# Kernel tuning notes

Measured on AMD Instinct MI355X. Metric: run time of the kernel, lower is better.

Reference implementation:

```python
import jax, jax.numpy as jnp
import numpy as np

GS = 7        # grid_size
NB = 2        # num_boxes
NC = 20       # num_classes
THR = 0.5     # NMS threshold (source default)
IMG = 448.0   # max_size used in _encode_outputs


def _nms_keep(boxes, scores, valid, thr):
    """Faithful port of the source's (inverted) greedy NMS.

    Picks the highest-score alive box, keeps it, then RETAINS only boxes
    with IoU >= thr against it (discarding low-overlap ones), repeating.
    Fixed-shape: returns a bool keep-mask of length N.
    """
    N = scores.shape[0]
    x1, y1, x2, y2 = boxes[:, 0], boxes[:, 1], boxes[:, 2], boxes[:, 3]
    areas = (x2 - x1) * (y2 - y1)
    neg = jnp.asarray(-1e30, scores.dtype)
    idx = jnp.arange(N)

    def step(carry, _):
        alive, keep = carry
        any_alive = jnp.any(alive)
        i = jnp.argmax(jnp.where(alive, scores, neg))
        keep = keep | ((idx == i) & any_alive)
        ix1 = jnp.maximum(x1, x1[i]); iy1 = jnp.maximum(y1, y1[i])
        ix2 = jnp.minimum(x2, x2[i]); iy2 = jnp.minimum(y2, y2[i])
        inter = jnp.clip(ix2 - ix1, 0) * jnp.clip(iy2 - iy1, 0)
        iou = inter / (areas[i] + areas - inter)
        new_alive = (alive & (iou >= thr)) & (idx != i)
        alive = jnp.where(any_alive, new_alive, alive)
        return (alive, keep), None

    (_, keep), _ = jax.lax.scan(step, (valid, jnp.zeros(N, bool)), None, length=N)
    return keep


def _forward(x, W, b):
    B = x.shape[0]
    out = (x @ W.T + b).reshape(B, GS, GS, 5 * NB + NC)  # (B,7,7,30)
    cell = 1.0 / GS
    g = jnp.arange(GS, dtype=out.dtype) * cell
    norm_x = g[None, None, :]   # varies along last grid axis (grid_x[r,c]=c)
    norm_y = g[None, :, None]

    labels = out[..., 5 * NB:]                                # (B,7,7,20)
    labels_proba = jnp.argmax(labels, -1).astype(out.dtype)   # class index

    N = B * GS * GS
    labels_flat = labels.reshape(N, NC)

    slot_boxes, slot_scores, slot_valid = [], [], []
    for off in range(0, 5 * NB, 5):
        bx = out[..., off:off + 4]
        sc = out[..., off + 5]                 # faithful off-by-one in source
        valid = (sc * labels_proba) > 0.5      # faithful score*class_index mask
        cx = bx[..., 0] * cell + norm_x
        cy = bx[..., 1] * cell + norm_y
        w_, h_ = bx[..., 2], bx[..., 3]
        X1 = cx - 0.5 * w_; Y1 = cy - 0.5 * h_
        X2 = cx + 0.5 * w_; Y2 = cy + 0.5 * h_
        # NMS applies xywh2xyxy AGAIN on already-xyxy boxes (faithful):
        bb = jnp.stack([X1 - X2 / 2, Y1 - Y2 / 2, X1 + X2 / 2, Y1 + Y2 / 2], -1)
        slot_boxes.append(bb.reshape(N, 4))
        slot_scores.append(sc.reshape(N))
        slot_valid.append(valid.reshape(N))

    boxes = jnp.stack(slot_boxes)     # (NB, N, 4)
    scores = jnp.stack(slot_scores)   # (NB, N)
    valid = jnp.stack(slot_valid)     # (NB, N)

    keep = jax.vmap(_nms_keep, in_axes=(0, 0, 0, None))(boxes, scores, valid, THR)

    labels_all = jnp.broadcast_to(labels_flat[None], (NB, N, NC))
    packed = jnp.concatenate([boxes * IMG, scores[..., None], labels_all], -1)
    return packed * keep[..., None].astype(packed.dtype)  # (NB, N, 25)


def setup_inputs() -> dict:
    key = jax.random.key(0)
    k1, k2, k3 = jax.random.split(key, 3)
    B = 64
    x = jax.random.normal(k1, (B, 2304), jnp.float32)
    W = jax.random.normal(k2, (1470, 2304), jnp.float32) * 0.02
    b = jax.random.normal(k3, (1470,), jnp.float32) * 0.01
    return {"x": x, "W": W, "b": b}


def reference(x, W, b):
    return _forward(x, W, b)
```

## Files before the change

kernel.cpp:

```cpp
#include <hip/hip_runtime.h>

#define B_     64
#define KDIM   2304
#define NCOL   1470
#define NCELL  3136
#define CPAD   1536
#define SPLITK 16
#define KCHUNK 144
#define NSTAGE 9
#define XS     68
#define WSD    100
#define NMS_T  1024
#define QMAX   4
#define OUTSZ  (2 * NCELL * 25)

__global__ __launch_bounds__(256) void gemm_splitk(
    const float* __restrict__ x, const float* __restrict__ W,
    float* __restrict__ partial, float* __restrict__ out)
{
    __shared__ float sx[2][16 * XS];
    __shared__ float sw[2][16 * WSD];

    const int t = threadIdx.x;

    {
        const int gt = (blockIdx.y * 16 + blockIdx.x) * 256 + t;
        if (gt < OUTSZ / 4)
            *(float4*)&out[gt * 4] = make_float4(0.f, 0.f, 0.f, 0.f);
    }

    const int c0  = blockIdx.x * 96;
    const int k0  = blockIdx.y * KCHUNK;
    const int r8  = (t >> 5) << 3;
    const int cgi = t & 31;
    const int kk0 = t & 15;
    const int g0  = t >> 4;

    float acc[8][3];
#pragma unroll
    for (int i = 0; i < 8; ++i)
#pragma unroll
        for (int j = 0; j < 3; ++j) acc[i][j] = 0.f;

    const float* wp[6];
#pragma unroll
    for (int p = 0; p < 6; ++p) {
        int gc = c0 + p * 16 + g0;
        if (gc >= NCOL) gc = NCOL - 1;
        wp[p] = W + (size_t)gc * KDIM + kk0;
    }

    float xr[4], wr[6];
    {
        const int kb = k0;
#pragma unroll
        for (int p = 0; p < 4; ++p) xr[p] = x[(p * 16 + g0) * KDIM + kb + kk0];
#pragma unroll
        for (int p = 0; p < 6; ++p) wr[p] = wp[p][kb];
#pragma unroll
        for (int p = 0; p < 4; ++p) sx[0][kk0 * XS + p * 16 + g0] = xr[p];
#pragma unroll
        for (int p = 0; p < 6; ++p) sw[0][kk0 * WSD + p * 16 + g0] = wr[p];
    }

    for (int s = 0; s < NSTAGE; ++s) {
        const int cb = s & 1;
        if (s + 1 < NSTAGE) {
            const int kb = k0 + ((s + 1) << 4);
#pragma unroll
            for (int p = 0; p < 4; ++p) xr[p] = x[(p * 16 + g0) * KDIM + kb + kk0];
#pragma unroll
            for (int p = 0; p < 6; ++p) wr[p] = wp[p][kb];
        }
        __syncthreads();
        const float* cx = sx[cb];
        const float* cw = sw[cb];
#pragma unroll
        for (int kk = 0; kk < 16; ++kk) {
            const float4 a0 = *(const float4*)&cx[kk * XS + r8];
            const float4 a1 = *(const float4*)&cx[kk * XS + r8 + 4];
            const float w0 = cw[kk * WSD + cgi];
            const float w1 = cw[kk * WSD + cgi + 32];
            const float w2 = cw[kk * WSD + cgi + 64];
            const float av[8] = {a0.x, a0.y, a0.z, a0.w, a1.x, a1.y, a1.z, a1.w};
#pragma unroll
            for (int i = 0; i < 8; ++i) {
                acc[i][0] = fmaf(av[i], w0, acc[i][0]);
                acc[i][1] = fmaf(av[i], w1, acc[i][1]);
                acc[i][2] = fmaf(av[i], w2, acc[i][2]);
            }
        }
        if (s + 1 < NSTAGE) {
#pragma unroll
            for (int p = 0; p < 4; ++p) sx[cb ^ 1][kk0 * XS + p * 16 + g0] = xr[p];
#pragma unroll
            for (int p = 0; p < 6; ++p) sw[cb ^ 1][kk0 * WSD + p * 16 + g0] = wr[p];
        }
    }

    float* pb = partial + (size_t)blockIdx.y * (B_ * CPAD) + c0 + cgi;
#pragma unroll
    for (int i = 0; i < 8; ++i)
#pragma unroll
        for (int p = 0; p < 3; ++p)
            pb[(size_t)(r8 + i) * CPAD + 32 * p] = acc[i][p];
}

__global__ __launch_bounds__(256) void combine_prep(
    const float* __restrict__ partial, const float* __restrict__ bias,
    float* __restrict__ labels, float* __restrict__ boxes,
    float* __restrict__ scores, int* __restrict__ valid)
{
    __shared__ float sa[8][30];
    const int t    = threadIdx.x;
    const int base = blockIdx.x * 8;

    if (t < 240) {
        const int n   = base + t / 30;
        const int col = t % 30;
        const int row = n / 49;
        const int cr  = (n % 49) * 30 + col;
        float s = 0.f;
#pragma unroll
        for (int k = 0; k < SPLITK; ++k)
            s += partial[(size_t)k * (B_ * CPAD) + (size_t)row * CPAD + cr];
        s += bias[cr];
        sa[t / 30][col] = s;
        if (col >= 10) labels[(size_t)n * 20 + (col - 10)] = s;
    }
    __syncthreads();

    if (t < 8) {
        const int n = base + t;
        const float* a = sa[t];
        float mv = a[10]; int mi = 0;
#pragma unroll
        for (int j = 1; j < 20; ++j) {
            float v = a[10 + j];
            if (v > mv) { mv = v; mi = j; }
        }
        const float lp = (float)mi;
        const int gx = n % 7, gy = (n / 7) % 7;
        const float cw = 1.0f / 7.0f;
        const float nx = (float)gx * cw, ny = (float)gy * cw;
#pragma unroll
        for (int sl = 0; sl < 2; ++sl) {
            const int off = 5 * sl;
            const float bx0 = a[off], bx1 = a[off + 1];
            const float w_ = a[off + 2], h_ = a[off + 3];
            const float sc = a[off + 5];
            const float cx = bx0 * cw + nx, cy = bx1 * cw + ny;
            const float X1 = cx - 0.5f * w_, Y1 = cy - 0.5f * h_;
            const float X2 = cx + 0.5f * w_, Y2 = cy + 0.5f * h_;
            const int m = sl * NCELL + n;
            boxes[m * 4 + 0] = X1 - 0.5f * X2;
            boxes[m * 4 + 1] = Y1 - 0.5f * Y2;
            boxes[m * 4 + 2] = X1 + 0.5f * X2;
            boxes[m * 4 + 3] = Y1 + 0.5f * Y2;
            scores[m] = sc;
            valid[m] = (sc * lp > 0.5f) ? 1 : 0;
        }
    }
}

__global__ __launch_bounds__(NMS_T) void nms_pick(
    const float* __restrict__ boxes, const float* __restrict__ scores,
    const int* __restrict__ valid, const float* __restrict__ labels,
    float* __restrict__ out)
{
    __shared__ float sX1[NCELL], sY1[NCELL], sX2[NCELL], sY2[NCELL];
    __shared__ float sSc[NCELL];
    __shared__ int   pickList[NCELL];
    __shared__ float rv[16];
    __shared__ int   rn[16];
    __shared__ int   pickN, npicks;

    const int slot = blockIdx.x;
    const int base = slot * NCELL;
    const int t = threadIdx.x;

    if (t == 0) npicks = 0;
    unsigned am = 0;
#pragma unroll
    for (int q = 0; q < QMAX; ++q) {
        const int n = t + q * NMS_T;
        if (n < NCELL) {
            const float4 bb = *(const float4*)&boxes[(size_t)(base + n) * 4];
            sX1[n] = bb.x; sY1[n] = bb.y; sX2[n] = bb.z; sY2[n] = bb.w;
            sSc[n] = scores[base + n];
            if (valid[base + n]) am |= 1u << q;
        }
    }
    __syncthreads();

    for (;;) {
        float bv = -1e30f; int bn = 0x7fffffff;
#pragma unroll
        for (int q = 0; q < QMAX; ++q)
            if ((am >> q) & 1u) {
                const int n = t + q * NMS_T;
                const float v = sSc[n];
                if (v > bv || (v == bv && n < bn)) { bv = v; bn = n; }
            }
#pragma unroll
        for (int o = 32; o > 0; o >>= 1) {
            const float ov = __shfl_down(bv, o);
            const int   on = __shfl_down(bn, o);
            if (ov > bv || (ov == bv && on < bn)) { bv = ov; bn = on; }
        }
        if ((t & 63) == 0) { rv[t >> 6] = bv; rn[t >> 6] = bn; }
        __syncthreads();
        if (t == 0) {
            float v2 = rv[0]; int n2 = rn[0];
#pragma unroll
            for (int q = 1; q < 16; ++q)
                if (rv[q] > v2 || (rv[q] == v2 && rn[q] < n2)) { v2 = rv[q]; n2 = rn[q]; }
            if (v2 == -1e30f) { pickN = -1; }
            else { pickN = n2; pickList[npicks++] = n2; }
        }
        __syncthreads();
        const int pn = pickN;
        if (pn < 0) break;
        const float px1 = sX1[pn], py1 = sY1[pn], px2 = sX2[pn], py2 = sY2[pn];
        const float pa = (px2 - px1) * (py2 - py1);

#pragma unroll
        for (int q = 0; q < QMAX; ++q)
            if ((am >> q) & 1u) {
                const int n = t + q * NMS_T;
                const float x1 = sX1[n], y1 = sY1[n], x2 = sX2[n], y2 = sY2[n];
                const float an = (x2 - x1) * (y2 - y1);
                const float ix1 = fmaxf(x1, px1), iy1 = fmaxf(y1, py1);
                const float ix2 = fminf(x2, px2), iy2 = fminf(y2, py2);
                const float inter = fmaxf(ix2 - ix1, 0.f) * fmaxf(iy2 - iy1, 0.f);
                const float iou = inter / (pa + an - inter);
                if (!(iou >= 0.5f) || n == pn) am &= ~(1u << q);
            }
    }

    const int np = npicks;
    for (int u = t; u < np * 25; u += NMS_T) {
        const int pi = u / 25;
        const int c  = u % 25;
        const int n  = pickList[pi];
        float v;
        if (c < 4)       v = (c == 0 ? sX1[n] : c == 1 ? sY1[n] : c == 2 ? sX2[n] : sY2[n]) * 448.0f;
        else if (c == 4) v = sSc[n];
        else             v = labels[(size_t)n * 20 + (c - 5)];
        out[(size_t)(base + n) * 25 + c] = v;
    }
}

extern "C" void kernel_launch(void* const* d_in, const int* in_sizes, int n_in,
                              void* d_out, int out_size, void* d_ws, size_t ws_size,
                              hipStream_t stream)
{
    const float* x = (const float*)d_in[0];
    const float* W = (const float*)d_in[1];
    const float* b = (const float*)d_in[2];
    float* out = (float*)d_out;

    float* ws      = (float*)d_ws;
    float* partial = ws;
    float* labels  = partial + (size_t)SPLITK * B_ * CPAD;
    float* boxes   = labels + (size_t)NCELL * 20;
    float* scores  = boxes + (size_t)NCELL * 8;
    int*   valid   = (int*)(scores + (size_t)NCELL * 2);

    hipLaunchKernelGGL(gemm_splitk, dim3(16, SPLITK), dim3(256), 0, stream,
                       x, W, partial, out);
    hipLaunchKernelGGL(combine_prep, dim3(NCELL / 8), dim3(256), 0, stream,
                       partial, b, labels, boxes, scores, valid);
    hipLaunchKernelGGL(nms_pick, dim3(2), dim3(NMS_T), 0, stream,
                       boxes, scores, valid, labels, out);
}
```

Measured before the change: 30.95 us.

## Fuse combine and NMS kernels using a global atomic counter barrier

Merges the combine/prep kernel and the NMS kernel into one launch. Every block increments a device-scope atomic counter after writing its boxes, and blocks 0 and 1 spin until all 392 blocks have arrived before running NMS. The NMS part now uses 256 threads with 13 cells per thread instead of 1024 threads with 4. This removes one kernel launch and its gap, but the spin-wait needs blocks 0 and 1 to stay resident alongside the rest, every block now carries the large NMS shared-memory allocation, and the NMS loop has less parallelism.

Result: slower. 61.14 us (+97.5%).

```diff
diff --git a/kernel.cpp b/kernel.cpp
--- a/kernel.cpp
+++ b/kernel.cpp
@@ -10,18 +10,21 @@
 #define NSTAGE 9
 #define XS     68
 #define WSD    100
-#define NMS_T  1024
-#define QMAX   4
+#define NBLK2  392
+#define NMS_T  256
+#define QMAX   13
 #define OUTSZ  (2 * NCELL * 25)
 
 __global__ __launch_bounds__(256) void gemm_splitk(
     const float* __restrict__ x, const float* __restrict__ W,
-    float* __restrict__ partial, float* __restrict__ out)
+    float* __restrict__ partial, float* __restrict__ out,
+    int* __restrict__ cnts)
 {
     __shared__ float sx[2][16 * XS];
     __shared__ float sw[2][16 * WSD];
 
     const int t = threadIdx.x;
+    if (blockIdx.x == 0 && blockIdx.y == 0 && t == 0) cnts[0] = 0;
 
     {
         const int gt = (blockIdx.y * 16 + blockIdx.x) * 256 + t;
@@ -106,12 +109,20 @@
             pb[(size_t)(r8 + i) * CPAD + 32 * p] = acc[i][p];
 }
 
-__global__ __launch_bounds__(256) void combine_prep(
+__global__ __launch_bounds__(256) void combine_nms(
     const float* __restrict__ partial, const float* __restrict__ bias,
     float* __restrict__ labels, float* __restrict__ boxes,
-    float* __restrict__ scores, int* __restrict__ valid)
+    float* __restrict__ scores, int* __restrict__ valid,
+    int* __restrict__ cnts, float* __restrict__ out)
 {
     __shared__ float sa[8][30];
+    __shared__ float sX1[NCELL], sY1[NCELL], sX2[NCELL], sY2[NCELL];
+    __shared__ float sSc[NCELL];
+    __shared__ int   pickList[NCELL];
+    __shared__ float rv[4];
+    __shared__ int   rn[4];
+    __shared__ int   pickN, npicks;
+
     const int t    = threadIdx.x;
     const int base = blockIdx.x * 8;
 
@@ -161,23 +172,22 @@
             valid[m] = (sc * lp > 0.5f) ? 1 : 0;
         }
     }
-}
-
-__global__ __launch_bounds__(NMS_T) void nms_pick(
-    const float* __restrict__ boxes, const float* __restrict__ scores,
-    const int* __restrict__ valid, const float* __restrict__ labels,
-    float* __restrict__ out)
-{
-    __shared__ float sX1[NCELL], sY1[NCELL], sX2[NCELL], sY2[NCELL];
-    __shared__ float sSc[NCELL];
-    __shared__ int   pickList[NCELL];
-    __shared__ float rv[16];
-    __shared__ int   rn[16];
-    __shared__ int   pickN, npicks;
+
+    __threadfence();
+    __syncthreads();
+    if (t == 0)
+        __hip_atomic_fetch_add(&cnts[0], 1, __ATOMIC_RELEASE, __HIP_MEMORY_SCOPE_AGENT);
+
+    if (blockIdx.x >= 2) return;
+
+    if (t == 0) {
+        while (__hip_atomic_load(&cnts[0], __ATOMIC_ACQUIRE, __HIP_MEMORY_SCOPE_AGENT) < NBLK2) {}
+    }
+    __syncthreads();
+    __threadfence();
 
     const int slot = blockIdx.x;
-    const int base = slot * NCELL;
-    const int t = threadIdx.x;
+    const int nb   = slot * NCELL;
 
     if (t == 0) npicks = 0;
     unsigned am = 0;
@@ -185,10 +195,10 @@
     for (int q = 0; q < QMAX; ++q) {
         const int n = t + q * NMS_T;
         if (n < NCELL) {
-            const float4 bb = *(const float4*)&boxes[(size_t)(base + n) * 4];
+            const float4 bb = *(const float4*)&boxes[(size_t)(nb + n) * 4];
             sX1[n] = bb.x; sY1[n] = bb.y; sX2[n] = bb.z; sY2[n] = bb.w;
-            sSc[n] = scores[base + n];
-            if (valid[base + n]) am |= 1u << q;
+            sSc[n] = scores[nb + n];
+            if (valid[nb + n]) am |= 1u << q;
         }
     }
     __syncthreads();
@@ -213,7 +223,7 @@
         if (t == 0) {
             float v2 = rv[0]; int n2 = rn[0];
 #pragma unroll
-            for (int q = 1; q < 16; ++q)
+            for (int q = 1; q < 4; ++q)
                 if (rv[q] > v2 || (rv[q] == v2 && rn[q] < n2)) { v2 = rv[q]; n2 = rn[q]; }
             if (v2 == -1e30f) { pickN = -1; }
             else { pickN = n2; pickList[npicks++] = n2; }
@@ -247,7 +257,7 @@
         if (c < 4)       v = (c == 0 ? sX1[n] : c == 1 ? sY1[n] : c == 2 ? sX2[n] : sY2[n]) * 448.0f;
         else if (c == 4) v = sSc[n];
         else             v = labels[(size_t)n * 20 + (c - 5)];
-        out[(size_t)(base + n) * 25 + c] = v;
+        out[(size_t)(nb + n) * 25 + c] = v;
     }
 }
 
@@ -266,11 +276,10 @@
     float* boxes   = labels + (size_t)NCELL * 20;
     float* scores  = boxes + (size_t)NCELL * 8;
     int*   valid   = (int*)(scores + (size_t)NCELL * 2);
+    int*   cnts    = valid + (size_t)NCELL * 2;
 
     hipLaunchKernelGGL(gemm_splitk, dim3(16, SPLITK), dim3(256), 0, stream,
-                       x, W, partial, out);
-    hipLaunchKernelGGL(combine_prep, dim3(NCELL / 8), dim3(256), 0, stream,
-                       partial, b, labels, boxes, scores, valid);
-    hipLaunchKernelGGL(nms_pick, dim3(2), dim3(NMS_T), 0, stream,
-                       boxes, scores, valid, labels, out);
+                       x, W, partial, out, cnts);
+    hipLaunchKernelGGL(combine_nms, dim3(NBLK2), dim3(256), 0, stream,
+                       partial, b, labels, boxes, scores, valid, cnts, out);
 }
```
